# Kernel optimization log

Hardware: AMD Instinct MI355X
Metric: run time of the kernel (lower is better)

Reference implementation:

```python
import jax, jax.numpy as jnp
import numpy as np

B, C, H, W = 4, 256, 224, 224
WH = WW = 8
SH = SW = 4
HEADS = 8
HD = C // HEADS
N = WH * WW
EPS = 1e-5


def _rel_index():
    coords = np.stack(np.meshgrid(np.arange(WH), np.arange(WW), indexing='ij')).reshape(2, -1)
    rel = (coords[:, :, None] - coords[:, None, :]).transpose(1, 2, 0).copy()
    rel[:, :, 0] += WH - 1
    rel[:, :, 1] += WW - 1
    rel[:, :, 0] *= 2 * WW - 1
    return rel.sum(-1)  # (N, N) int

REL_INDEX = _rel_index()


def _shift_mask(Hp, Wp):
    # Swin shift mask for one image: (nW, N, N) float, 0 or -100
    img = np.zeros((Hp, Wp))
    cnt = 0
    for a, b in [(0, Hp - WH), (Hp - WH, Hp - SH), (Hp - SH, Hp)]:
        for c, d in [(0, Wp - WW), (Wp - WW, Wp - SW), (Wp - SW, Wp)]:
            img[a:b, c:d] = cnt
            cnt += 1
    mw = img.reshape(Hp // WH, WH, Wp // WW, WW).transpose(0, 2, 1, 3).reshape(-1, N)
    diff = mw[:, None, :] - mw[:, :, None]  # [w, i, j] = mw[w,j] - mw[w,i]
    return np.where(diff != 0, np.float32(-100.0), np.float32(0.0)).astype(np.float32)


def _ln(x, w, b):
    m = jnp.mean(x, axis=-1, keepdims=True)
    v = jnp.mean(jnp.square(x - m), axis=-1, keepdims=True)
    return (x - m) * jax.lax.rsqrt(v + EPS) * w + b


def setup_inputs() -> dict:
    key = jax.random.key(0)
    ks = jax.random.split(key, 8)
    num_rel = (2 * WH - 1) * (2 * WW - 1)
    return {
        'x': jax.random.normal(ks[0], (B, C, H, W), dtype=jnp.float32),
        'qkv_w': jax.random.normal(ks[1], (3 * C, C), dtype=jnp.float32) * 0.02,
        'proj_w': jax.random.normal(ks[2], (C, C), dtype=jnp.float32) * 0.02,
        'proj_b': jnp.zeros((C,), dtype=jnp.float32),
        'rpb_table': jax.random.normal(ks[3], (num_rel, HEADS), dtype=jnp.float32) * 0.02,
        'norm1_w': jnp.ones((C,), dtype=jnp.float32),
        'norm1_b': jnp.zeros((C,), dtype=jnp.float32),
        'norm2_w': jnp.ones((C,), dtype=jnp.float32),
        'norm2_b': jnp.zeros((C,), dtype=jnp.float32),
        'mlp_w1': jax.random.normal(ks[4], (4 * C, C), dtype=jnp.float32) * 0.02,
        'mlp_b1': jnp.zeros((4 * C,), dtype=jnp.float32),
        'mlp_w2': jax.random.normal(ks[5], (C, 4 * C), dtype=jnp.float32) * 0.02,
        'mlp_b2': jnp.zeros((C,), dtype=jnp.float32),
    }


def reference(x, qkv_w, proj_w, proj_b, rpb_table, norm1_w, norm1_b,
              norm2_w, norm2_b, mlp_w1, mlp_b1, mlp_w2, mlp_b2):
    Bx, Cx, Hx, Wx = x.shape
    pad_h = (WH - Hx % WH) % WH
    pad_w = (WW - Wx % WW) % WW
    if pad_h or pad_w:
        x = jnp.pad(x, ((0, 0), (0, 0), (0, pad_h), (0, pad_w)))
    Hp, Wp = Hx + pad_h, Wx + pad_w
    x = jnp.transpose(x, (0, 2, 3, 1))                    # BHWC
    x = jnp.roll(x, (-SH, -SW), axis=(1, 2))
    nW = (Hp // WH) * (Wp // WW)
    # window partition -> (B*nW, N, C), batch-major
    xw = x.reshape(Bx, Hp // WH, WH, Wp // WW, WW, Cx)
    xw = jnp.transpose(xw, (0, 1, 3, 2, 4, 5)).reshape(-1, N, Cx)

    # ----- windowed attention -----
    h = _ln(xw, norm1_w, norm1_b)
    qkv = (h @ qkv_w.T).reshape(-1, N, 3, HEADS, HD)
    qkv = jnp.transpose(qkv, (2, 0, 3, 1, 4))             # (3, Bw, heads, N, hd)
    q, k, v = qkv[0], qkv[1], qkv[2]
    attn = jnp.einsum('bhnd,bhmd->bhnm', q, k) * (1.0 / HD ** 0.5)
    bias = jnp.transpose(rpb_table[REL_INDEX.reshape(-1)].reshape(N, N, HEADS), (2, 0, 1))
    attn = attn + bias[None]
    # faithful to torch: repeat_interleave(B, dim=0) -> window-major mask ordering
    mask = jnp.asarray(_shift_mask(Hp, Wp))               # (nW, N, N)
    attn = attn + jnp.repeat(mask, Bx, axis=0)[:, None]
    attn = jax.nn.softmax(attn, axis=-1)
    out = jnp.einsum('bhnm,bhmd->bhnd', attn, v)
    out = jnp.transpose(out, (0, 2, 1, 3)).reshape(-1, N, Cx)
    out = out @ proj_w.T + proj_b
    xw = xw + out

    # ----- MLP -----
    h = _ln(xw, norm2_w, norm2_b)
    h = jax.nn.gelu(h @ mlp_w1.T + mlp_b1, approximate=False) @ mlp_w2.T + mlp_b2
    xw = xw + h

    # window reverse, un-shift, un-pad
    x = xw.reshape(Bx, Hp // WH, Wp // WW, WH, WW, Cx)
    x = jnp.transpose(x, (0, 1, 3, 2, 4, 5)).reshape(Bx, Hp, Wp, Cx)
    x = jnp.roll(x, (SH, SW), axis=(1, 2))
    x = x[:, :Hx, :Wx, :]
    return jnp.transpose(x, (0, 3, 1, 2))
```

## Files before the change

### kernel.cpp

```cpp
#include <hip/hip_runtime.h>

typedef unsigned short u16;
typedef unsigned int   u32;
typedef __attribute__((ext_vector_type(8))) __bf16 bf16x8;
typedef __attribute__((ext_vector_type(4))) float  f32x4;
typedef __attribute__((ext_vector_type(4))) u16    u16x4;
typedef __attribute__((ext_vector_type(8))) u16    u16x8;

#define DEV __device__ __forceinline__

DEV u16 f2b(float f) {
  union { float f; u32 u; } a; a.f = f;
  const u32 u = a.u;
  return (u16)((u + 0x7fffu + ((u >> 16) & 1u)) >> 16);
}

DEV float gelu_fast(float x) {
  const float x2 = x * x;
  const float t  = __builtin_fmaf(0.1029430f, x2, 2.3022150f);
  const float e  = __builtin_exp2f(x * t);
  const float r  = __builtin_amdgcn_rcpf(1.0f + e);
  return __builtin_fmaf(-x, r, x);
}

DEV void gload16(const void* g, void* l) {
  __builtin_amdgcn_global_load_lds(
      (const __attribute__((address_space(1))) void*)g,
      (__attribute__((address_space(3))) void*)l, 16, 0, 0);
}

__global__ __launch_bounds__(256)
void conv_weights(const float* __restrict__ qkvw, const float* __restrict__ projw,
                  const float* __restrict__ w1,   const float* __restrict__ w2,
                  u16* __restrict__ dq, u16* __restrict__ dp,
                  u16* __restrict__ d1, u16* __restrict__ d2) {
  const int t = blockIdx.x * 256 + threadIdx.x;
  if (t < 196608)      dq[t]          = f2b(qkvw[t]);
  else if (t < 262144) dp[t - 196608] = f2b(projw[t - 196608]);
  else if (t < 524288) d1[t - 262144] = f2b(w1[t - 262144]);
  else                 d2[t - 524288] = f2b(w2[t - 524288]);
}

__global__ __launch_bounds__(256)
void ln1_win(const float* __restrict__ x, const float* __restrict__ w1,
             const float* __restrict__ b1, u16* __restrict__ hout,
             float* __restrict__ xwout) {
  __shared__ float xt[64 * 257];
  __shared__ float smean[256], srstd[256];
  const int tid = threadIdx.x, lane = tid & 63, wv = tid >> 6;
  const int g = blockIdx.x;
  const int b = g / 196, rem = g % 196;
  const int wh = rem / 7, wg = rem % 7;
  const int base_r = b * 784 + wh * 28 + wg * 4;
  const int pr = tid >> 5, pc = tid & 31;
  int hp = wh * 8 + 4 + pr; if (hp >= 224) hp -= 224;
  int wp = wg * 32 + 4 + pc; if (wp >= 224) wp -= 224;
  const long roff = (long)b * 256 * 50176 + hp * 224 + wp;

  float s = 0.f, q = 0.f;
  for (int cc = 0; cc < 4; ++cc) {
#pragma unroll 8
    for (int i = 0; i < 64; ++i) {
      const int c = cc * 64 + i;
      const float v = x[(long)c * 50176 + roff];
      xt[i * 257 + tid] = v;
      s += v; q += v * v;
    }
    __syncthreads();
#pragma unroll 8
    for (int jj = 0; jj < 64; ++jj) {
      const int p = jj * 4 + wv;
      const int m = (base_r + ((p & 31) >> 3)) * 64 + (p >> 5) * 8 + (p & 7);
      xwout[(long)m * 256 + cc * 64 + lane] = xt[lane * 257 + p];
    }
    __syncthreads();
  }
  const float mean = s * (1.f / 256.f);
  smean[tid] = mean;
  srstd[tid] = rsqrtf(q * (1.f / 256.f) - mean * mean + 1e-5f);
  __syncthreads();

  float wr_[4], br_[4];
#pragma unroll
  for (int cc = 0; cc < 4; ++cc) { wr_[cc] = w1[cc * 64 + lane]; br_[cc] = b1[cc * 64 + lane]; }
#pragma unroll 2
  for (int jj = 0; jj < 64; ++jj) {
    const int p = jj * 4 + wv;
    const int m = (base_r + ((p & 31) >> 3)) * 64 + (p >> 5) * 8 + (p & 7);
    const float mu = smean[p], rs = srstd[p];
#pragma unroll
    for (int cc = 0; cc < 4; ++cc) {
      const float v = xwout[(long)m * 256 + cc * 64 + lane];
      hout[(long)m * 256 + cc * 64 + lane] = f2b((v - mu) * rs * wr_[cc] + br_[cc]);
    }
  }
}

template<int EPI, int NCOL>
__global__ __launch_bounds__(512, 2)
void gemm_bt(const u16* __restrict__ A, const u16* __restrict__ Bw, const int K,
             float* __restrict__ fout, const float* __restrict__ bias,
             u16* __restrict__ bout,
             const float* __restrict__ lnw, const float* __restrict__ lnb) {
  __shared__ __align__(16) u16 smem[65536];
  u16* sA0 = smem;
  u16* sB0 = smem + 16384;
  u16* sA1 = smem + 32768;
  u16* sB1 = smem + 49152;

  const int tid  = threadIdx.x;
  const int lane = tid & 63;
  const int wid  = tid >> 6;
  const int wr   = wid >> 2;
  const int wc   = wid & 3;

  const int nwg = gridDim.x;
  const int bid = blockIdx.x;
  const int wg  = (bid & 7) * (nwg >> 3) + (bid >> 3);
  const int row_blk = wg / NCOL;
  const int col_blk = wg - row_blk * NCOL;
  const int row0 = row_blk * 256;
  const int col0 = col_blk * 256;

  const f32x4 vzero = {0.f, 0.f, 0.f, 0.f};
  f32x4 acc[8][4];
#pragma unroll
  for (int i = 0; i < 8; ++i)
#pragma unroll
    for (int j = 0; j < 4; ++j) acc[i][j] = vzero;

  const int lrow = lane >> 3;
  const int lcol = ((lane & 7) << 3) ^ (lane & 56);
  const int l15  = lane & 15;
  const int l4   = lane >> 4;
  const int ksw  = (lane & 7) << 3;

  const u16* pA = A  + (long)(row0 + lrow) * K + lcol;
  const u16* pB = Bw + (long)(col0 + lrow) * K + lcol;

#define STAGE_TILE(KT, DA, DB)                                       \
  {                                                                  \
    _Pragma("unroll")                                                \
    for (int ch = 0; ch < 4; ++ch) {                                 \
      const int rr = ch * 64 + wid * 8;                              \
      gload16(pA + (long)rr * K + (KT), (DA) + rr * 64);             \
      gload16(pB + (long)rr * K + (KT), (DB) + rr * 64);             \
    }                                                                \
  }

#define COMPUTE_TILE(SA, SB, SWAP)                                                      \
  {                                                                                     \
    _Pragma("unroll")                                                                   \
    for (int kk = 0; kk < 2; ++kk) {                                                    \
      bf16x8 af[8], bfv[4];                                                             \
      _Pragma("unroll")                                                                 \
      for (int mi = 0; mi < 8; ++mi)                                                    \
        af[mi] = *(const bf16x8*)((SA) + (wr * 128 + mi * 16 + l15) * 64 +              \
                                  ((kk * 32 + l4 * 8) ^ ksw));                          \
      _Pragma("unroll")                                                                 \
      for (int nj = 0; nj < 4; ++nj)                                                    \
        bfv[nj] = *(const bf16x8*)((SB) + (wc * 64 + nj * 16 + l15) * 64 +              \
                                   ((kk * 32 + l4 * 8) ^ ksw));                         \
      _Pragma("unroll")                                                                 \
      for (int mi = 0; mi < 8; ++mi)                                                    \
        _Pragma("unroll")                                                               \
        for (int nj = 0; nj < 4; ++nj) {                                                \
          if (SWAP)                                                                     \
            acc[mi][nj] = __builtin_amdgcn_mfma_f32_16x16x32_bf16(bfv[nj], af[mi],      \
                                                                  acc[mi][nj], 0, 0, 0);\
          else                                                                          \
            acc[mi][nj] = __builtin_amdgcn_mfma_f32_16x16x32_bf16(af[mi], bfv[nj],      \
                                                                  acc[mi][nj], 0, 0, 0);\
        }                                                                               \
    }                                                                                   \
  }

#define KLOOP(SWAP)                                                  \
  {                                                                  \
    const int nt = K >> 6;                                           \
    STAGE_TILE(0, sA0, sB0);                                         \
    int cur = 0;                                                     \
    for (int t = 0; t < nt; ++t) {                                   \
      u16* cA = cur ? sA1 : sA0;                                     \
      u16* cB = cur ? sB1 : sB0;                                     \
      u16* nA = cur ? sA0 : sA1;                                     \
      u16* nB = cur ? sB0 : sB1;                                     \
      if (t + 1 < nt) {                                              \
        STAGE_TILE((t + 1) << 6, nA, nB);                            \
        asm volatile("s_waitcnt vmcnt(8)" ::: "memory");             \
      } else {                                                       \
        asm volatile("s_waitcnt vmcnt(0)" ::: "memory");             \
      }                                                              \
      __builtin_amdgcn_s_barrier();                                  \
      asm volatile("" ::: "memory");                                 \
      COMPUTE_TILE(cA, cB, SWAP);                                    \
      asm volatile("" ::: "memory");                                 \
      __builtin_amdgcn_s_barrier();                                  \
      cur ^= 1;                                                      \
    }                                                                \
  }

  if (EPI == 0 && col_blk == 2) {
    KLOOP(0);
#pragma unroll
    for (int mi = 0; mi < 8; ++mi) {
      const int mb = row0 + wr * 128 + mi * 16 + (l4 << 2);
      const int rrg = mb >> 6, ii = mb & 63;
#pragma unroll
      for (int nj = 0; nj < 4; ++nj) {
        const int n = 512 + wc * 64 + nj * 16 + l15;
        const int hh = (n >> 5) & 7, d = n & 31;
        u16x4 p;
#pragma unroll
        for (int reg = 0; reg < 4; ++reg) p[reg] = f2b(acc[mi][nj][reg]);
        *(u16x4*)(bout + 102760448L + (long)((rrg * 8 + hh) * 32 + d) * 64 + ii) = p;
      }
    }
    return;
  }

  KLOOP(1);

#undef STAGE_TILE
#undef COMPUTE_TILE
#undef KLOOP

  if (EPI == 0) {
#pragma unroll
    for (int mi = 0; mi < 8; ++mi) {
      const int m = row0 + wr * 128 + mi * 16 + l15;
      const int rr = m >> 6, ii = m & 63;
#pragma unroll
      for (int nj = 0; nj < 4; ++nj) {
        const int n = col0 + wc * 64 + nj * 16 + (l4 << 2);
        const int s = n >> 8, hh = (n >> 5) & 7, d = n & 31;
        u16x4 p;
#pragma unroll
        for (int reg = 0; reg < 4; ++reg) p[reg] = f2b(acc[mi][nj][reg]);
        *(u16x4*)(bout + (long)s * 51380224L +
                  (long)((rr * 8 + hh) * 64 + ii) * 32 + d) = p;
      }
    }
  } else if (EPI == 1) {
    f32x4 b4[4];
#pragma unroll
    for (int nj = 0; nj < 4; ++nj)
      b4[nj] = *(const f32x4*)(bias + wc * 64 + nj * 16 + (l4 << 2));
    float sS[8], sQ[8];
#pragma unroll
    for (int mi = 0; mi < 8; ++mi) {
      const int m = row0 + wr * 128 + mi * 16 + l15;
      float* yrow = fout + (long)m * 256;
      float s = 0.f, q = 0.f;
#pragma unroll
      for (int nj = 0; nj < 4; ++nj) {
        const int n = wc * 64 + nj * 16 + (l4 << 2);
        f32x4 o = *(f32x4*)(yrow + n);
#pragma unroll
        for (int reg = 0; reg < 4; ++reg) {
          o[reg] += acc[mi][nj][reg] + b4[nj][reg];
          s += o[reg]; q += o[reg] * o[reg];
        }
        *(f32x4*)(yrow + n) = o;
        acc[mi][nj] = o;
      }
      s += __shfl_xor(s, 16); s += __shfl_xor(s, 32);
      q += __shfl_xor(q, 16); q += __shfl_xor(q, 32);
      sS[mi] = s; sQ[mi] = q;
    }
    float* ps = (float*)smem;
    float* pq = ps + 1024;
    __syncthreads();
    if (lane < 16) {
#pragma unroll
      for (int mi = 0; mi < 8; ++mi) {
        const int idx = ((wr * 8 + mi) * 16 + l15) * 4 + wc;
        ps[idx] = sS[mi]; pq[idx] = sQ[mi];
      }
    }
    __syncthreads();
#pragma unroll
    for (int mi = 0; mi < 8; ++mi) {
      const int m = row0 + wr * 128 + mi * 16 + l15;
      const int base = ((wr * 8 + mi) * 16 + l15) * 4;
      const float S = ps[base] + ps[base + 1] + ps[base + 2] + ps[base + 3];
      const float Q = pq[base] + pq[base + 1] + pq[base + 2] + pq[base + 3];
      const float mean = S * (1.f / 256.f);
      const float rstd = rsqrtf(Q * (1.f / 256.f) - mean * mean + 1e-5f);
#pragma unroll
      for (int nj = 0; nj < 4; ++nj) {
        const int n = wc * 64 + nj * 16 + (l4 << 2);
        const f32x4 w4 = *(const f32x4*)(lnw + n);
        const f32x4 c4 = *(const f32x4*)(lnb + n);
        u16x4 p;
#pragma unroll
        for (int reg = 0; reg < 4; ++reg)
          p[reg] = f2b((acc[mi][nj][reg] - mean) * rstd * w4[reg] + c4[reg]);
        *(u16x4*)(bout + (long)m * 256 + n) = p;
      }
    }
  } else if (EPI == 3) {
    f32x4 b4[4];
#pragma unroll
    for (int nj = 0; nj < 4; ++nj)
      b4[nj] = *(const f32x4*)(bias + wc * 64 + nj * 16 + (l4 << 2));
#pragma unroll
    for (int mi = 0; mi < 8; ++mi) {
      const int m = row0 + wr * 128 + mi * 16 + l15;
      float* yrow = fout + (long)m * 256;
#pragma unroll
      for (int nj = 0; nj < 4; ++nj) {
        const int n = wc * 64 + nj * 16 + (l4 << 2);
        f32x4 o = *(f32x4*)(yrow + n);
#pragma unroll
        for (int reg = 0; reg < 4; ++reg) o[reg] += acc[mi][nj][reg] + b4[nj][reg];
        *(f32x4*)(yrow + n) = o;
      }
    }
  } else if (EPI == 2) {
    f32x4 b4[4];
#pragma unroll
    for (int nj = 0; nj < 4; ++nj)
      b4[nj] = *(const f32x4*)(bias + col0 + wc * 64 + nj * 16 + (l4 << 2));
#pragma unroll
    for (int mi = 0; mi < 8; ++mi) {
      const int m = row0 + wr * 128 + mi * 16 + l15;
#pragma unroll
      for (int nj = 0; nj < 4; ++nj) {
        const int n = col0 + wc * 64 + nj * 16 + (l4 << 2);
        u16x4 p;
#pragma unroll
        for (int reg = 0; reg < 4; ++reg)
          p[reg] = f2b(gelu_fast(acc[mi][nj][reg] + b4[nj][reg]));
        *(u16x4*)(bout + (long)m * 1024 + n) = p;
      }
    }
  }
}

__global__ __launch_bounds__(256)
void attn_win(const u16* __restrict__ qkv, const float* __restrict__ rpb,
              u16* __restrict__ aout) {
  __shared__ u16 Pl[4][4096];
  __shared__ float srpb[1800];
  const int tid = threadIdx.x, lane = tid & 63, wv = tid >> 6;
  const int bid = blockIdx.x;
  const int r = bid >> 1;
  const int h = (bid & 1) * 4 + wv;
  for (int i = tid; i < 1800; i += 256) srpb[i] = rpb[i];
  __syncthreads();

  const int midx = r >> 2;
  const int wh = midx / 28, ww = midx % 28;
  const int l15 = lane & 15, l4 = lane >> 4;

  u16* Pw = &Pl[wv][0];
  const long hb = (long)(r * 8 + h) * 2048;
  const u16* qh = qkv + hb;
  const u16* kh = qkv + 51380224 + hb;
  const u16* vh = qkv + 102760448 + hb;

  int rj[4], cj[4], labj[4];
#pragma unroll
  for (int nj = 0; nj < 4; ++nj) {
    const int j = nj * 16 + l15;
    rj[nj] = j >> 3; cj[nj] = j & 7;
    const int hp = wh * 8 + rj[nj], wp = ww * 8 + cj[nj];
    const int lh = (hp < 216) ? 0 : ((hp < 220) ? 1 : 2);
    const int lw = (wp < 216) ? 0 : ((wp < 220) ? 1 : 2);
    labj[nj] = lh * 3 + lw;
  }

  const f32x4 vzero = {0.f, 0.f, 0.f, 0.f};

  bf16x8 qf[4], kf[4];
#pragma unroll
  for (int mi = 0; mi < 4; ++mi)
    qf[mi] = *(const bf16x8*)(qh + (mi * 16 + l15) * 32 + l4 * 8);
#pragma unroll
  for (int nj = 0; nj < 4; ++nj)
    kf[nj] = *(const bf16x8*)(kh + (nj * 16 + l15) * 32 + l4 * 8);

  f32x4 S[4][4];
#pragma unroll
  for (int mi = 0; mi < 4; ++mi)
#pragma unroll
    for (int nj = 0; nj < 4; ++nj)
      S[mi][nj] = __builtin_amdgcn_mfma_f32_16x16x32_bf16(qf[mi], kf[nj], vzero, 0, 0, 0);

#pragma unroll
  for (int mi = 0; mi < 4; ++mi)
#pragma unroll
    for (int reg = 0; reg < 4; ++reg) {
      const int i = mi * 16 + (l4 << 2) + reg;
      const int ri = i >> 3, ci = i & 7;
      const int hp = wh * 8 + ri, wp = ww * 8 + ci;
      const int lh = (hp < 216) ? 0 : ((hp < 220) ? 1 : 2);
      const int lw = (wp < 216) ? 0 : ((wp < 220) ? 1 : 2);
      const int li = lh * 3 + lw;
      float v[4];
#pragma unroll
      for (int nj = 0; nj < 4; ++nj) {
        const int idx = (ri - rj[nj] + 7) * 15 + (ci - cj[nj] + 7);
        v[nj] = S[mi][nj][reg] * 0.17677669529663687f + srpb[idx * 8 + h]
              + ((li != labj[nj]) ? -100.0f : 0.0f);
      }
      float mx = fmaxf(fmaxf(v[0], v[1]), fmaxf(v[2], v[3]));
      mx = fmaxf(mx, __shfl_xor(mx, 1));
      mx = fmaxf(mx, __shfl_xor(mx, 2));
      mx = fmaxf(mx, __shfl_xor(mx, 4));
      mx = fmaxf(mx, __shfl_xor(mx, 8));
      float sum = 0.f;
#pragma unroll
      for (int nj = 0; nj < 4; ++nj) { v[nj] = __expf(v[nj] - mx); sum += v[nj]; }
      sum += __shfl_xor(sum, 1);
      sum += __shfl_xor(sum, 2);
      sum += __shfl_xor(sum, 4);
      sum += __shfl_xor(sum, 8);
      const float rinv = __builtin_amdgcn_rcpf(sum);
      const int sw = (i & 7) << 3;
#pragma unroll
      for (int nj = 0; nj < 4; ++nj)
        Pw[i * 64 + ((nj * 16 + l15) ^ sw)] = f2b(v[nj] * rinv);
    }

  f32x4 OT[2][4];
#pragma unroll
  for (int td = 0; td < 2; ++td)
#pragma unroll
    for (int ti = 0; ti < 4; ++ti) OT[td][ti] = vzero;

  const int rsw = (l15 & 7) << 3;
#pragma unroll
  for (int kk = 0; kk < 2; ++kk) {
    bf16x8 pf[4], vf[2];
#pragma unroll
    for (int ti = 0; ti < 4; ++ti)
      pf[ti] = *(const bf16x8*)(Pw + (ti * 16 + l15) * 64 + ((kk * 32 + l4 * 8) ^ rsw));
#pragma unroll
    for (int td = 0; td < 2; ++td)
      vf[td] = *(const bf16x8*)(vh + (td * 16 + l15) * 64 + kk * 32 + l4 * 8);
#pragma unroll
    for (int td = 0; td < 2; ++td)
#pragma unroll
      for (int ti = 0; ti < 4; ++ti)
        OT[td][ti] = __builtin_amdgcn_mfma_f32_16x16x32_bf16(vf[td], pf[ti], OT[td][ti], 0, 0, 0);
  }

#pragma unroll
  for (int td = 0; td < 2; ++td)
#pragma unroll
    for (int ti = 0; ti < 4; ++ti) {
      const int i = ti * 16 + l15;
      const int d0 = td * 16 + (l4 << 2);
      u16x4 p;
#pragma unroll
      for (int reg = 0; reg < 4; ++reg) p[reg] = f2b(OT[td][ti][reg]);
      *(u16x4*)(aout + (long)(r * 64 + i) * 256 + h * 32 + d0) = p;
    }
}

__global__ __launch_bounds__(256)
void unwin(const float* __restrict__ y, float* __restrict__ out) {
  __shared__ float xt[64 * 257];
  const int tid = threadIdx.x, lane = tid & 63, wv = tid >> 6;
  const int g = blockIdx.x;
  const int b = g / 196, rem = g % 196;
  const int wh = rem / 7, wg = rem % 7;
  const int base_r = b * 784 + wh * 28 + wg * 4;
  const int pr = tid >> 5, pc = tid & 31;
  int hp = wh * 8 + 4 + pr; if (hp >= 224) hp -= 224;
  int wp = wg * 32 + 4 + pc; if (wp >= 224) wp -= 224;
  const long woff = (long)b * 256 * 50176 + hp * 224 + wp;

  for (int cc = 0; cc < 4; ++cc) {
#pragma unroll 8
    for (int jj = 0; jj < 64; ++jj) {
      const int p = jj * 4 + wv;
      const int m = (base_r + ((p & 31) >> 3)) * 64 + (p >> 5) * 8 + (p & 7);
      xt[lane * 257 + p] = y[(long)m * 256 + cc * 64 + lane];
    }
    __syncthreads();
#pragma unroll 8
    for (int i = 0; i < 64; ++i)
      out[(long)(cc * 64 + i) * 50176 + woff] = xt[i * 257 + tid];
    __syncthreads();
  }
}

extern "C" void kernel_launch(void* const* d_in, const int* in_sizes, int n_in,
                              void* d_out, int out_size, void* d_ws, size_t ws_size,
                              hipStream_t stream) {
  (void)in_sizes; (void)n_in; (void)out_size; (void)ws_size;
  const float* x     = (const float*)d_in[0];
  const float* qkvw  = (const float*)d_in[1];
  const float* projw = (const float*)d_in[2];
  const float* projb = (const float*)d_in[3];
  const float* rpb   = (const float*)d_in[4];
  const float* n1w   = (const float*)d_in[5];
  const float* n1b   = (const float*)d_in[6];
  const float* n2w   = (const float*)d_in[7];
  const float* n2b   = (const float*)d_in[8];
  const float* w1    = (const float*)d_in[9];
  const float* b1    = (const float*)d_in[10];
  const float* w2    = (const float*)d_in[11];
  const float* b2    = (const float*)d_in[12];

  char* ws = (char*)d_ws;
  u16*   hbuf   = (u16*)(ws);
  u16*   qkvb   = (u16*)(ws + 102760448);
  u16*   abuf   = (u16*)(ws + 411041792);
  float* ybuf   = (float*)(ws + 513802240);
  u16*   hidb   = (u16*)(ws + 102760448);
  u16*   qkvwb  = (u16*)(ws + 719323136);
  u16*   projwb = (u16*)(ws + 719716352);
  u16*   w1b    = (u16*)(ws + 719847424);
  u16*   w2b    = (u16*)(ws + 720371712);

  conv_weights<<<3072, 256, 0, stream>>>(qkvw, projw, w1, w2, qkvwb, projwb, w1b, w2b);
  ln1_win<<<784, 256, 0, stream>>>(x, n1w, n1b, hbuf, ybuf);
  gemm_bt<0, 3><<<2352, 512, 0, stream>>>(hbuf, qkvwb, 256, nullptr, nullptr, qkvb, nullptr, nullptr);
  attn_win<<<6272, 256, 0, stream>>>(qkvb, rpb, abuf);
  gemm_bt<1, 1><<<784, 512, 0, stream>>>(abuf, projwb, 256, ybuf, projb, hbuf, n2w, n2b);
  gemm_bt<2, 4><<<3136, 512, 0, stream>>>(hbuf, w1b, 256, nullptr, b1, hidb, nullptr, nullptr);
  gemm_bt<3, 1><<<784, 512, 0, stream>>>(hidb, w2b, 1024, ybuf, b2, nullptr, nullptr, nullptr);
  unwin<<<784, 256, 0, stream>>>(ybuf, (float*)d_out);
}
```

Before: 1.244 ms.

## Use 1024-thread GEMM blocks and fuse window-reverse store into MLP2 epilogue

```diff
diff --git a/kernel.cpp b/kernel.cpp
--- a/kernel.cpp
+++ b/kernel.cpp
@@ -97,11 +97,12 @@
 }
 
 template<int EPI, int NCOL>
-__global__ __launch_bounds__(512, 2)
+__global__ __launch_bounds__(1024, 4)
 void gemm_bt(const u16* __restrict__ A, const u16* __restrict__ Bw, const int K,
              float* __restrict__ fout, const float* __restrict__ bias,
              u16* __restrict__ bout,
-             const float* __restrict__ lnw, const float* __restrict__ lnb) {
+             const float* __restrict__ lnw, const float* __restrict__ lnb,
+             float* __restrict__ oout) {
   __shared__ __align__(16) u16 smem[65536];
   u16* sA0 = smem;
   u16* sB0 = smem + 16384;
@@ -111,8 +112,8 @@
   const int tid  = threadIdx.x;
   const int lane = tid & 63;
   const int wid  = tid >> 6;
-  const int wr   = wid >> 2;
-  const int wc   = wid & 3;
+  const int wrr  = wid >> 2;
+  const int wcc  = wid & 3;
 
   const int nwg = gridDim.x;
   const int bid = blockIdx.x;
@@ -123,9 +124,9 @@
   const int col0 = col_blk * 256;
 
   const f32x4 vzero = {0.f, 0.f, 0.f, 0.f};
-  f32x4 acc[8][4];
-#pragma unroll
-  for (int i = 0; i < 8; ++i)
+  f32x4 acc[4][4];
+#pragma unroll
+  for (int i = 0; i < 4; ++i)
 #pragma unroll
     for (int j = 0; j < 4; ++j) acc[i][j] = vzero;
 
@@ -135,34 +136,33 @@
   const int l4   = lane >> 4;
   const int ksw  = (lane & 7) << 3;
 
-  const u16* pA = A  + (long)(row0 + lrow) * K + lcol;
-  const u16* pB = Bw + (long)(col0 + lrow) * K + lcol;
-
-#define STAGE_TILE(KT, DA, DB)                                       \
-  {                                                                  \
-    _Pragma("unroll")                                                \
-    for (int ch = 0; ch < 4; ++ch) {                                 \
-      const int rr = ch * 64 + wid * 8;                              \
-      gload16(pA + (long)rr * K + (KT), (DA) + rr * 64);             \
-      gload16(pB + (long)rr * K + (KT), (DB) + rr * 64);             \
-    }                                                                \
+  const u16* pA = A  + (long)(row0 + wid * 8 + lrow) * K + lcol;
+  const u16* pB = Bw + (long)(col0 + wid * 8 + lrow) * K + lcol;
+
+#define STAGE_TILE(KT, DA, DB)                                          \
+  {                                                                     \
+    _Pragma("unroll")                                                   \
+    for (int ch = 0; ch < 2; ++ch) {                                    \
+      gload16(pA + (long)(ch * 128) * K + (KT), (DA) + (ch * 128 + wid * 8) * 64); \
+      gload16(pB + (long)(ch * 128) * K + (KT), (DB) + (ch * 128 + wid * 8) * 64); \
+    }                                                                   \
   }
 
 #define COMPUTE_TILE(SA, SB, SWAP)                                                      \
   {                                                                                     \
     _Pragma("unroll")                                                                   \
     for (int kk = 0; kk < 2; ++kk) {                                                    \
-      bf16x8 af[8], bfv[4];                                                             \
+      bf16x8 af[4], bfv[4];                                                             \
       _Pragma("unroll")                                                                 \
-      for (int mi = 0; mi < 8; ++mi)                                                    \
-        af[mi] = *(const bf16x8*)((SA) + (wr * 128 + mi * 16 + l15) * 64 +              \
+      for (int mi = 0; mi < 4; ++mi)                                                    \
+        af[mi] = *(const bf16x8*)((SA) + (wrr * 64 + mi * 16 + l15) * 64 +              \
                                   ((kk * 32 + l4 * 8) ^ ksw));                          \
       _Pragma("unroll")                                                                 \
       for (int nj = 0; nj < 4; ++nj)                                                    \
-        bfv[nj] = *(const bf16x8*)((SB) + (wc * 64 + nj * 16 + l15) * 64 +              \
+        bfv[nj] = *(const bf16x8*)((SB) + (wcc * 64 + nj * 16 + l15) * 64 +             \
                                    ((kk * 32 + l4 * 8) ^ ksw));                         \
       _Pragma("unroll")                                                                 \
-      for (int mi = 0; mi < 8; ++mi)                                                    \
+      for (int mi = 0; mi < 4; ++mi)                                                    \
         _Pragma("unroll")                                                               \
         for (int nj = 0; nj < 4; ++nj) {                                                \
           if (SWAP)                                                                     \
@@ -187,7 +187,7 @@
       u16* nB = cur ? sB0 : sB1;                                     \
       if (t + 1 < nt) {                                              \
         STAGE_TILE((t + 1) << 6, nA, nB);                            \
-        asm volatile("s_waitcnt vmcnt(8)" ::: "memory");             \
+        asm volatile("s_waitcnt vmcnt(4)" ::: "memory");             \
       } else {                                                       \
         asm volatile("s_waitcnt vmcnt(0)" ::: "memory");             \
       }                                                              \
@@ -203,12 +203,12 @@
   if (EPI == 0 && col_blk == 2) {
     KLOOP(0);
 #pragma unroll
-    for (int mi = 0; mi < 8; ++mi) {
-      const int mb = row0 + wr * 128 + mi * 16 + (l4 << 2);
+    for (int mi = 0; mi < 4; ++mi) {
+      const int mb = row0 + wrr * 64 + mi * 16 + (l4 << 2);
       const int rrg = mb >> 6, ii = mb & 63;
 #pragma unroll
       for (int nj = 0; nj < 4; ++nj) {
-        const int n = 512 + wc * 64 + nj * 16 + l15;
+        const int n = 512 + wcc * 64 + nj * 16 + l15;
         const int hh = (n >> 5) & 7, d = n & 31;
         u16x4 p;
 #pragma unroll
@@ -227,12 +227,12 @@
 
   if (EPI == 0) {
 #pragma unroll
-    for (int mi = 0; mi < 8; ++mi) {
-      const int m = row0 + wr * 128 + mi * 16 + l15;
+    for (int mi = 0; mi < 4; ++mi) {
+      const int m = row0 + wrr * 64 + mi * 16 + l15;
       const int rr = m >> 6, ii = m & 63;
 #pragma unroll
       for (int nj = 0; nj < 4; ++nj) {
-        const int n = col0 + wc * 64 + nj * 16 + (l4 << 2);
+        const int n = col0 + wcc * 64 + nj * 16 + (l4 << 2);
         const int s = n >> 8, hh = (n >> 5) & 7, d = n & 31;
         u16x4 p;
 #pragma unroll
@@ -245,16 +245,16 @@
     f32x4 b4[4];
 #pragma unroll
     for (int nj = 0; nj < 4; ++nj)
-      b4[nj] = *(const f32x4*)(bias + wc * 64 + nj * 16 + (l4 << 2));
-    float sS[8], sQ[8];
-#pragma unroll
-    for (int mi = 0; mi < 8; ++mi) {
-      const int m = row0 + wr * 128 + mi * 16 + l15;
+      b4[nj] = *(const f32x4*)(bias + wcc * 64 + nj * 16 + (l4 << 2));
+    float sS[4], sQ[4];
+#pragma unroll
+    for (int mi = 0; mi < 4; ++mi) {
+      const int m = row0 + wrr * 64 + mi * 16 + l15;
       float* yrow = fout + (long)m * 256;
       float s = 0.f, q = 0.f;
 #pragma unroll
       for (int nj = 0; nj < 4; ++nj) {
-        const int n = wc * 64 + nj * 16 + (l4 << 2);
+        const int n = wcc * 64 + nj * 16 + (l4 << 2);
         f32x4 o = *(f32x4*)(yrow + n);
 #pragma unroll
         for (int reg = 0; reg < 4; ++reg) {
@@ -273,23 +273,23 @@
     __syncthreads();
     if (lane < 16) {
 #pragma unroll
-      for (int mi = 0; mi < 8; ++mi) {
-        const int idx = ((wr * 8 + mi) * 16 + l15) * 4 + wc;
+      for (int mi = 0; mi < 4; ++mi) {
+        const int idx = ((wrr * 4 + mi) * 16 + l15) * 4 + wcc;
         ps[idx] = sS[mi]; pq[idx] = sQ[mi];
       }
     }
     __syncthreads();
 #pragma unroll
-    for (int mi = 0; mi < 8; ++mi) {
-      const int m = row0 + wr * 128 + mi * 16 + l15;
-      const int base = ((wr * 8 + mi) * 16 + l15) * 4;
+    for (int mi = 0; mi < 4; ++mi) {
+      const int m = row0 + wrr * 64 + mi * 16 + l15;
+      const int base = ((wrr * 4 + mi) * 16 + l15) * 4;
       const float S = ps[base] + ps[base + 1] + ps[base + 2] + ps[base + 3];
       const float Q = pq[base] + pq[base + 1] + pq[base + 2] + pq[base + 3];
       const float mean = S * (1.f / 256.f);
       const float rstd = rsqrtf(Q * (1.f / 256.f) - mean * mean + 1e-5f);
 #pragma unroll
       for (int nj = 0; nj < 4; ++nj) {
-        const int n = wc * 64 + nj * 16 + (l4 << 2);
+        const int n = wcc * 64 + nj * 16 + (l4 << 2);
         const f32x4 w4 = *(const f32x4*)(lnw + n);
         const f32x4 c4 = *(const f32x4*)(lnb + n);
         u16x4 p;
@@ -303,31 +303,63 @@
     f32x4 b4[4];
 #pragma unroll
     for (int nj = 0; nj < 4; ++nj)
-      b4[nj] = *(const f32x4*)(bias + wc * 64 + nj * 16 + (l4 << 2));
-#pragma unroll
-    for (int mi = 0; mi < 8; ++mi) {
-      const int m = row0 + wr * 128 + mi * 16 + l15;
-      float* yrow = fout + (long)m * 256;
-#pragma unroll
-      for (int nj = 0; nj < 4; ++nj) {
-        const int n = wc * 64 + nj * 16 + (l4 << 2);
-        f32x4 o = *(f32x4*)(yrow + n);
-#pragma unroll
-        for (int reg = 0; reg < 4; ++reg) o[reg] += acc[mi][nj][reg] + b4[nj][reg];
-        *(f32x4*)(yrow + n) = o;
+      b4[nj] = *(const f32x4*)(bias + wcc * 64 + nj * 16 + (l4 << 2));
+#pragma unroll
+    for (int mi = 0; mi < 4; ++mi) {
+      const int m = row0 + wrr * 64 + mi * 16 + l15;
+      const float* yrow = fout + (long)m * 256;
+#pragma unroll
+      for (int nj = 0; nj < 4; ++nj) {
+        const int n = wcc * 64 + nj * 16 + (l4 << 2);
+        const f32x4 yv = *(const f32x4*)(yrow + n);
+#pragma unroll
+        for (int reg = 0; reg < 4; ++reg)
+          acc[mi][nj][reg] += yv[reg] + b4[nj][reg];
+      }
+    }
+    const int g = row0 >> 8;
+    const int b = g / 196, rem = g % 196;
+    const int wh = rem / 7, wg2 = rem % 7;
+    float* tp = (float*)smem;
+    const int pidx = tid & 255, cgrp = tid >> 8;
+    const int pr = pidx >> 5, pc = pidx & 31;
+    int hp = wh * 8 + 4 + pr; if (hp >= 224) hp -= 224;
+    int wp = wg2 * 32 + 4 + pc; if (wp >= 224) wp -= 224;
+    float* ob = oout + (long)b * 256 * 50176 + hp * 224 + wp;
+    const int pxr = 4 * (pr * 8 + (pc & 7)) + (pc >> 3);
+#pragma unroll
+    for (int cc = 0; cc < 4; ++cc) {
+      __syncthreads();
+      if (wcc == cc) {
+#pragma unroll
+        for (int mi = 0; mi < 4; ++mi) {
+          const int pxw = (4 * (mi * 16 + l15) + wrr) ^ l4;
+#pragma unroll
+          for (int nj = 0; nj < 4; ++nj)
+#pragma unroll
+            for (int reg = 0; reg < 4; ++reg)
+              tp[(nj * 16 + (l4 << 2) + reg) * 256 + pxw] = acc[mi][nj][reg];
+        }
+      }
+      __syncthreads();
+#pragma unroll 4
+      for (int j = 0; j < 16; ++j) {
+        const int c_local = cgrp * 16 + j;
+        ob[(long)(cc * 64 + c_local) * 50176] =
+            tp[c_local * 256 + (pxr ^ ((j >> 2) & 3))];
       }
     }
   } else if (EPI == 2) {
     f32x4 b4[4];
 #pragma unroll
     for (int nj = 0; nj < 4; ++nj)
-      b4[nj] = *(const f32x4*)(bias + col0 + wc * 64 + nj * 16 + (l4 << 2));
-#pragma unroll
-    for (int mi = 0; mi < 8; ++mi) {
-      const int m = row0 + wr * 128 + mi * 16 + l15;
-#pragma unroll
-      for (int nj = 0; nj < 4; ++nj) {
-        const int n = col0 + wc * 64 + nj * 16 + (l4 << 2);
+      b4[nj] = *(const f32x4*)(bias + col0 + wcc * 64 + nj * 16 + (l4 << 2));
+#pragma unroll
+    for (int mi = 0; mi < 4; ++mi) {
+      const int m = row0 + wrr * 64 + mi * 16 + l15;
+#pragma unroll
+      for (int nj = 0; nj < 4; ++nj) {
+        const int n = col0 + wcc * 64 + nj * 16 + (l4 << 2);
         u16x4 p;
 #pragma unroll
         for (int reg = 0; reg < 4; ++reg)
@@ -458,34 +490,6 @@
       for (int reg = 0; reg < 4; ++reg) p[reg] = f2b(OT[td][ti][reg]);
       *(u16x4*)(aout + (long)(r * 64 + i) * 256 + h * 32 + d0) = p;
     }
-}
-
-__global__ __launch_bounds__(256)
-void unwin(const float* __restrict__ y, float* __restrict__ out) {
-  __shared__ float xt[64 * 257];
-  const int tid = threadIdx.x, lane = tid & 63, wv = tid >> 6;
-  const int g = blockIdx.x;
-  const int b = g / 196, rem = g % 196;
-  const int wh = rem / 7, wg = rem % 7;
-  const int base_r = b * 784 + wh * 28 + wg * 4;
-  const int pr = tid >> 5, pc = tid & 31;
-  int hp = wh * 8 + 4 + pr; if (hp >= 224) hp -= 224;
-  int wp = wg * 32 + 4 + pc; if (wp >= 224) wp -= 224;
-  const long woff = (long)b * 256 * 50176 + hp * 224 + wp;
-
-  for (int cc = 0; cc < 4; ++cc) {
-#pragma unroll 8
-    for (int jj = 0; jj < 64; ++jj) {
-      const int p = jj * 4 + wv;
-      const int m = (base_r + ((p & 31) >> 3)) * 64 + (p >> 5) * 8 + (p & 7);
-      xt[lane * 257 + p] = y[(long)m * 256 + cc * 64 + lane];
-    }
-    __syncthreads();
-#pragma unroll 8
-    for (int i = 0; i < 64; ++i)
-      out[(long)(cc * 64 + i) * 50176 + woff] = xt[i * 257 + tid];
-    __syncthreads();
-  }
 }
 
 extern "C" void kernel_launch(void* const* d_in, const int* in_sizes, int n_in,
@@ -519,10 +523,9 @@
 
   conv_weights<<<3072, 256, 0, stream>>>(qkvw, projw, w1, w2, qkvwb, projwb, w1b, w2b);
   ln1_win<<<784, 256, 0, stream>>>(x, n1w, n1b, hbuf, ybuf);
-  gemm_bt<0, 3><<<2352, 512, 0, stream>>>(hbuf, qkvwb, 256, nullptr, nullptr, qkvb, nullptr, nullptr);
+  gemm_bt<0, 3><<<2352, 1024, 0, stream>>>(hbuf, qkvwb, 256, nullptr, nullptr, qkvb, nullptr, nullptr, nullptr);
   attn_win<<<6272, 256, 0, stream>>>(qkvb, rpb, abuf);
-  gemm_bt<1, 1><<<784, 512, 0, stream>>>(abuf, projwb, 256, ybuf, projb, hbuf, n2w, n2b);
-  gemm_bt<2, 4><<<3136, 512, 0, stream>>>(hbuf, w1b, 256, nullptr, b1, hidb, nullptr, nullptr);
-  gemm_bt<3, 1><<<784, 512, 0, stream>>>(hidb, w2b, 1024, ybuf, b2, nullptr, nullptr, nullptr);
-  unwin<<<784, 256, 0, stream>>>(ybuf, (float*)d_out);
-}
+  gemm_bt<1, 1><<<784, 1024, 0, stream>>>(abuf, projwb, 256, ybuf, projb, hbuf, n2w, n2b, nullptr);
+  gemm_bt<2, 4><<<3136, 1024, 0, stream>>>(hbuf, w1b, 256, nullptr, b1, hidb, nullptr, nullptr, nullptr);
+  gemm_bt<3, 1><<<784, 1024, 0, stream>>>(hidb, w2b, 1024, ybuf, b2, nullptr, nullptr, nullptr, (float*)d_out);
+}
```

Result: faster. 1.125 ms (-9.6%).
